# Optimization experiments

Measured on AMD Instinct MI355X. Metric: run time of the kernel, lower is better.

Reference implementation:

```python
import jax, jax.numpy as jnp
import numpy as np

N_HEAD = 16
N_KV = 4
HEAD_DIM = 128
WINDOW = 1024
SINK = 4
THETA = 10000.0


def _rope_cos_sin(T, dim, theta, dtype):
    inv_freq = 1.0 / (theta ** (jnp.arange(0, dim, 2, dtype=jnp.float32) / dim))
    t = jnp.arange(T, dtype=jnp.float32)
    ang = jnp.outer(t, inv_freq)  # [T, dim/2]
    return jnp.cos(ang).astype(dtype), jnp.sin(ang).astype(dtype)


def _apply_rope(x, cos, sin):
    # x: [B, H, T, D]; cos/sin: [T, D/2]
    d2 = x.shape[-1] // 2
    x1, x2 = x[..., :d2], x[..., d2:]
    return jnp.concatenate([x1 * cos - x2 * sin, x2 * cos + x1 * sin], axis=-1)


def setup_inputs() -> dict:
    key = jax.random.key(0)
    ks = jax.random.split(key, 5)
    B, T, C = 2, 2048, 2048
    x = jax.random.normal(ks[0], (B, T, C), dtype=jnp.float32)
    s = 0.02
    wq = jax.random.normal(ks[1], (C, C), dtype=jnp.float32) * s
    wk = jax.random.normal(ks[2], (N_KV * HEAD_DIM, C), dtype=jnp.float32) * s
    wv = jax.random.normal(ks[3], (N_KV * HEAD_DIM, C), dtype=jnp.float32) * s
    wo = jax.random.normal(ks[4], (C, C), dtype=jnp.float32) * s
    return {"x": x, "wq": wq, "wk": wk, "wv": wv, "wo": wo}


def reference(x, wq, wk, wv, wo):
    B, T, C = x.shape
    # QKV projections (Linear with weight [out, in], no bias)
    q = (x @ wq.T).reshape(B, T, N_HEAD, HEAD_DIM).transpose(0, 2, 1, 3)  # [B,H,T,D]
    k = (x @ wk.T).reshape(B, T, N_KV, HEAD_DIM).transpose(0, 2, 1, 3)    # [B,Hkv,T,D]
    v = (x @ wv.T).reshape(B, T, N_KV, HEAD_DIM).transpose(0, 2, 1, 3)

    cos, sin = _rope_cos_sin(T, HEAD_DIM, THETA, x.dtype)
    q = _apply_rope(q, cos, sin)
    k = _apply_rope(k, cos, sin)

    # GQA: repeat kv heads to match query heads (repeat_interleave on head dim)
    rep = N_HEAD // N_KV
    k = jnp.repeat(k, rep, axis=1)
    v = jnp.repeat(v, rep, axis=1)

    # causal + sliding window + attention sink mask
    i = jnp.arange(T)[:, None]
    j = jnp.arange(T)[None, :]
    allowed = (j <= i) & (((i - j) <= WINDOW) | (j < SINK))
    bias = jnp.where(allowed, 0.0, -jnp.inf).astype(x.dtype)  # [T,T]

    scale = 1.0 / np.sqrt(HEAD_DIM)
    att = jnp.einsum("bhqd,bhkd->bhqk", q, k) * scale + bias
    att = jax.nn.softmax(att, axis=-1)
    y = jnp.einsum("bhqk,bhkd->bhqd", att, v)  # [B,H,T,D]
    y = y.transpose(0, 2, 1, 3).reshape(B, T, C)
    return y @ wo.T
```

## Files before the change

### kernel.cpp

```cpp
#include <hip/hip_runtime.h>
#include <hip/hip_bf16.h>

typedef __bf16 bf16x8 __attribute__((ext_vector_type(8)));
typedef __bf16 bf16x4 __attribute__((ext_vector_type(4)));
typedef float  f32x4  __attribute__((ext_vector_type(4)));
typedef unsigned int uint4v __attribute__((ext_vector_type(4)));

#define NB     2
#define TT     2048
#define CC     2048
#define NH     16
#define NKV    4
#define HD     128
#define WIN    1024
#define SINKN  4
#define QSCALE 0.08838834764831845f

__device__ __forceinline__ void lds_load16(const void* g, void* l) {
    __builtin_amdgcn_global_load_lds(
        (__attribute__((address_space(1))) void*)const_cast<void*>(g),
        (__attribute__((address_space(3))) void*)l, 16, 0, 0);
}

__device__ __forceinline__ unsigned pack2bf(float a, float b) {
    __bf16 x = (__bf16)a, y = (__bf16)b;
    unsigned short ux = __builtin_bit_cast(unsigned short, x);
    unsigned short uy = __builtin_bit_cast(unsigned short, y);
    return (unsigned)ux | ((unsigned)uy << 16);
}

__global__ void cvt_kernel(const float* __restrict__ in, __bf16* __restrict__ out, int n) {
    int idx = (blockIdx.x * blockDim.x + threadIdx.x) * 4;
    const int stride = gridDim.x * blockDim.x * 4;
    for (; idx < n; idx += stride) {
        const float4 v = *(const float4*)(in + idx);
        bf16x4 o;
        o[0] = (__bf16)v.x; o[1] = (__bf16)v.y; o[2] = (__bf16)v.z; o[3] = (__bf16)v.w;
        *(bf16x4*)(out + idx) = o;
    }
}

__global__ void cvt_w_kernel(const float* __restrict__ wq, const float* __restrict__ wk,
                             const float* __restrict__ wv, const float* __restrict__ wo,
                             __bf16* __restrict__ out) {
    int idx = (blockIdx.x * blockDim.x + threadIdx.x) * 4;
    const int stride = gridDim.x * blockDim.x * 4;
    for (; idx < 10485760; idx += stride) {
        const float* src; int off;
        if (idx < 4194304)      { src = wq; off = idx; }
        else if (idx < 5242880) { src = wk; off = idx - 4194304; }
        else if (idx < 6291456) { src = wv; off = idx - 5242880; }
        else                    { src = wo; off = idx - 6291456; }
        const float4 v = *(const float4*)(src + off);
        bf16x4 o;
        o[0] = (__bf16)v.x; o[1] = (__bf16)v.y; o[2] = (__bf16)v.z; o[3] = (__bf16)v.w;
        *(bf16x4*)(out + idx) = o;
    }
}

__global__ void rope_table_kernel(float* __restrict__ cosT, float* __restrict__ sinT) {
    const int i = blockIdx.x * blockDim.x + threadIdx.x;
    const int t = i >> 6, d = i & 63;
    const float inv_freq = 1.0f / powf(10000.0f, (float)d * (1.0f / 64.0f));
    const float ang = (float)t * inv_freq;
    cosT[i] = cosf(ang);
    sinT[i] = sinf(ang);
}

__global__ void rope_scatter_kernel(const __bf16* __restrict__ qkv,
                                    const float* __restrict__ cosT,
                                    const float* __restrict__ sinT,
                                    __bf16* __restrict__ Qo,
                                    __bf16* __restrict__ Ko) {
    const int m = blockIdx.x;
    const int b = m >> 11, t = m & 2047;
    const __bf16* row = qkv + (size_t)m * 3072;
    for (int p = threadIdx.x; p < 1280; p += 256) {
        const int d = p & 63;
        const float c = cosT[t * 64 + d], s = sinT[t * 64 + d];
        if (p < 1024) {
            const int hh = p >> 6;
            const float x1 = (float)row[hh * 128 + d];
            const float x2 = (float)row[hh * 128 + d + 64];
            __bf16* o = Qo + ((size_t)(b * NH + hh) * TT + t) * HD;
            o[d]      = (__bf16)((x1 * c - x2 * s) * QSCALE);
            o[d + 64] = (__bf16)((x2 * c + x1 * s) * QSCALE);
        } else {
            const int g = (p - 1024) >> 6;
            const float x1 = (float)row[2048 + g * 128 + d];
            const float x2 = (float)row[2048 + g * 128 + d + 64];
            __bf16* o = Ko + ((size_t)(b * NKV + g) * TT + t) * HD;
            o[d]      = (__bf16)(x1 * c - x2 * s);
            o[d + 64] = (__bf16)(x2 * c + x1 * s);
        }
    }
}

__global__ void v_transpose_kernel(const __bf16* __restrict__ qkv, __bf16* __restrict__ Vt) {
    __shared__ __bf16 tile[64][72];
    const int bkv = blockIdx.z;
    const int b = bkv >> 2, g = bkv & 3;
    const int t0 = blockIdx.x << 6, d0 = blockIdx.y << 6;
    const int r = threadIdx.x >> 2, cg = threadIdx.x & 3;
    const __bf16* src = qkv + (size_t)(b * TT + t0 + r) * 3072 + 2560 + g * 128 + d0 + cg * 16;
    *(bf16x8*)&tile[r][cg * 16]     = *(const bf16x8*)src;
    *(bf16x8*)&tile[r][cg * 16 + 8] = *(const bf16x8*)(src + 8);
    __syncthreads();
    __bf16* dst = Vt + ((size_t)bkv * HD + d0 + r) * TT + t0 + cg * 16;
    bf16x8 o0, o1;
#pragma unroll
    for (int c2 = 0; c2 < 8; ++c2) {
        o0[c2] = tile[cg * 16 + c2][r];
        o1[c2] = tile[cg * 16 + 8 + c2][r];
    }
    *(bf16x8*)dst = o0;
    *(bf16x8*)(dst + 8) = o1;
}

template <int OUT_BF16>
__global__ __launch_bounds__(512, 2) void gemm_bt8(const __bf16* __restrict__ A,
                                                   const __bf16* __restrict__ Bm,
                                                   void* __restrict__ C,
                                                   int M, int N, int K) {
    __shared__ __align__(16) __bf16 lA[2][256 * 64];
    __shared__ __align__(16) __bf16 lB[2][256 * 64];
    const int tid = threadIdx.x;
    const int lane = tid & 63;
    const int w = tid >> 6;
    const int wm = w >> 2, wn = w & 3;
    const int nbn = N >> 8;
    const int bm = blockIdx.x / nbn, bn = blockIdx.x % nbn;
    const int m0 = bm << 8, n0 = bn << 8;
    const int lr = lane & 15, lh = lane >> 4;
    const int NT = K >> 6;

    auto stageA = [&](int kt, int buf, int i) {
        const int d = i * 8192 + tid * 16;
        const int row = d >> 7;
        const int colb = (d & 127) ^ ((row & 7) << 4);
        lds_load16(A + (size_t)(m0 + row) * K + kt * 64 + (colb >> 1),
                   (char*)lA[buf] + i * 8192 + w * 1024);
    };
    auto stageB = [&](int kt, int buf, int i) {
        const int d = i * 8192 + tid * 16;
        const int row = d >> 7;
        const int colb = (d & 127) ^ ((row & 7) << 4);
        lds_load16(Bm + (size_t)(n0 + row) * K + kt * 64 + (colb >> 1),
                   (char*)lB[buf] + i * 8192 + w * 1024);
    };

    f32x4 acc[8][4] = {};

#pragma unroll
    for (int i = 0; i < 4; ++i) stageA(0, 0, i);
#pragma unroll
    for (int i = 0; i < 4; ++i) stageB(0, 0, i);
    asm volatile("s_waitcnt vmcnt(0)" ::: "memory");
    __syncthreads();

    for (int kt = 0; kt < NT; ++kt) {
        const int cur = kt & 1, nxt = cur ^ 1;
        const bool pf = (kt + 1 < NT);
        const char* bA = (const char*)lA[cur];
        const char* bB = (const char*)lB[cur];

        bf16x8 aF[4][2], b0[2][2], b1[2][2];
#pragma unroll
        for (int mf = 0; mf < 4; ++mf)
#pragma unroll
            for (int ks = 0; ks < 2; ++ks) {
                const int row = wm * 128 + mf * 16 + lr;
                const int cb = (ks * 64 + lh * 16) ^ ((row & 7) << 4);
                aF[mf][ks] = *(const bf16x8*)(bA + row * 128 + cb);
            }
#pragma unroll
        for (int nf = 0; nf < 2; ++nf)
#pragma unroll
            for (int ks = 0; ks < 2; ++ks) {
                const int row = wn * 64 + nf * 16 + lr;
                const int cb = (ks * 64 + lh * 16) ^ ((row & 7) << 4);
                b0[nf][ks] = *(const bf16x8*)(bB + row * 128 + cb);
            }
        if (pf) { stageA(kt + 1, nxt, 0); stageA(kt + 1, nxt, 1); stageA(kt + 1, nxt, 2); stageA(kt + 1, nxt, 3); }
        __builtin_amdgcn_s_setprio(1);
#pragma unroll
        for (int mf = 0; mf < 4; ++mf)
#pragma unroll
            for (int nf = 0; nf < 2; ++nf)
#pragma unroll
                for (int ks = 0; ks < 2; ++ks)
                    acc[mf][nf] = __builtin_amdgcn_mfma_f32_16x16x32_bf16(aF[mf][ks], b0[nf][ks], acc[mf][nf], 0, 0, 0);
        __builtin_amdgcn_s_setprio(0);

#pragma unroll
        for (int nf = 0; nf < 2; ++nf)
#pragma unroll
            for (int ks = 0; ks < 2; ++ks) {
                const int row = wn * 64 + 32 + nf * 16 + lr;
                const int cb = (ks * 64 + lh * 16) ^ ((row & 7) << 4);
                b1[nf][ks] = *(const bf16x8*)(bB + row * 128 + cb);
            }
        if (pf) { stageB(kt + 1, nxt, 0); stageB(kt + 1, nxt, 1); stageB(kt + 1, nxt, 2); stageB(kt + 1, nxt, 3); }
        __builtin_amdgcn_s_setprio(1);
#pragma unroll
        for (int mf = 0; mf < 4; ++mf)
#pragma unroll
            for (int nf = 0; nf < 2; ++nf)
#pragma unroll
                for (int ks = 0; ks < 2; ++ks)
                    acc[mf][nf + 2] = __builtin_amdgcn_mfma_f32_16x16x32_bf16(aF[mf][ks], b1[nf][ks], acc[mf][nf + 2], 0, 0, 0);
        __builtin_amdgcn_s_setprio(0);

#pragma unroll
        for (int mf = 0; mf < 4; ++mf)
#pragma unroll
            for (int ks = 0; ks < 2; ++ks) {
                const int row = wm * 128 + 64 + mf * 16 + lr;
                const int cb = (ks * 64 + lh * 16) ^ ((row & 7) << 4);
                aF[mf][ks] = *(const bf16x8*)(bA + row * 128 + cb);
            }
        __builtin_amdgcn_s_setprio(1);
#pragma unroll
        for (int mf = 0; mf < 4; ++mf)
#pragma unroll
            for (int nf = 0; nf < 2; ++nf)
#pragma unroll
                for (int ks = 0; ks < 2; ++ks)
                    acc[mf + 4][nf] = __builtin_amdgcn_mfma_f32_16x16x32_bf16(aF[mf][ks], b0[nf][ks], acc[mf + 4][nf], 0, 0, 0);
        __builtin_amdgcn_s_setprio(0);

        __builtin_amdgcn_s_setprio(1);
#pragma unroll
        for (int mf = 0; mf < 4; ++mf)
#pragma unroll
            for (int nf = 0; nf < 2; ++nf)
#pragma unroll
                for (int ks = 0; ks < 2; ++ks)
                    acc[mf + 4][nf + 2] = __builtin_amdgcn_mfma_f32_16x16x32_bf16(aF[mf][ks], b1[nf][ks], acc[mf + 4][nf + 2], 0, 0, 0);
        __builtin_amdgcn_s_setprio(0);

        asm volatile("s_waitcnt vmcnt(0)" ::: "memory");
        __syncthreads();
    }

#pragma unroll
    for (int mf = 0; mf < 8; ++mf)
#pragma unroll
        for (int nf = 0; nf < 4; ++nf)
#pragma unroll
            for (int r = 0; r < 4; ++r) {
                const size_t row = m0 + wm * 128 + mf * 16 + lh * 4 + r;
                const size_t col = n0 + wn * 64 + nf * 16 + lr;
                if (OUT_BF16) ((__bf16*)C)[row * N + col] = (__bf16)acc[mf][nf][r];
                else          ((float*)C)[row * N + col]  = acc[mf][nf][r];
            }
}

template <int OUT_BF16>
__global__ __launch_bounds__(256, 2) void gemm_bt(const __bf16* __restrict__ A,
                                                  const __bf16* __restrict__ Bm,
                                                  void* __restrict__ C,
                                                  int M, int N, int K) {
    __shared__ __align__(16) __bf16 lA[128 * 32];
    __shared__ __align__(16) __bf16 lB[128 * 32];
    const int tid = threadIdx.x;
    const int lane = tid & 63;
    const int w = tid >> 6;
    const int wr = w >> 1, wc = w & 1;
    const int nbn = N >> 7;
    const int bm = blockIdx.x / nbn, bn = blockIdx.x % nbn;
    const int m0 = bm << 7, n0 = bn << 7;
    const int lr = lane & 15, lk = (lane >> 4) << 3;
    f32x4 acc[4][4] = {};

    for (int k0 = 0; k0 < K; k0 += 32) {
        __syncthreads();
#pragma unroll
        for (int L = 0; L < 2; ++L) {
            const int o = L * 4096 + w * 1024 + lane * 16;
            const int row = o >> 6, col = (o & 63) >> 1;
            lds_load16(A + (size_t)(m0 + row) * K + k0 + col, (char*)lA + L * 4096 + w * 1024);
            lds_load16(Bm + (size_t)(n0 + row) * K + k0 + col, (char*)lB + L * 4096 + w * 1024);
        }
        asm volatile("s_waitcnt vmcnt(0)" ::: "memory");
        __syncthreads();

        bf16x8 af[4], bfr[4];
#pragma unroll
        for (int t = 0; t < 4; ++t) {
            af[t]  = *(const bf16x8*)&lA[(wr * 64 + t * 16 + lr) * 32 + lk];
            bfr[t] = *(const bf16x8*)&lB[(wc * 64 + t * 16 + lr) * 32 + lk];
        }
#pragma unroll
        for (int mt = 0; mt < 4; ++mt)
#pragma unroll
            for (int nt = 0; nt < 4; ++nt)
                acc[mt][nt] = __builtin_amdgcn_mfma_f32_16x16x32_bf16(af[mt], bfr[nt], acc[mt][nt], 0, 0, 0);
    }

    const int r0 = (lane >> 4) * 4;
#pragma unroll
    for (int mt = 0; mt < 4; ++mt)
#pragma unroll
        for (int nt = 0; nt < 4; ++nt)
#pragma unroll
            for (int r = 0; r < 4; ++r) {
                const size_t row = m0 + wr * 64 + mt * 16 + r0 + r;
                const size_t col = n0 + wc * 64 + nt * 16 + lr;
                if (OUT_BF16) ((__bf16*)C)[row * N + col] = (__bf16)acc[mt][nt][r];
                else          ((float*)C)[row * N + col]  = acc[mt][nt][r];
            }
}

__global__ __launch_bounds__(512, 4) void attn_kernel(const __bf16* __restrict__ Q,
                                                      const __bf16* __restrict__ Kg,
                                                      const __bf16* __restrict__ Vt,
                                                      __bf16* __restrict__ Y) {
    const int qt2 = 63 - blockIdx.x;
    const int kv = blockIdx.y, b = blockIdx.z;
    const int q0 = qt2 << 5;
    const int tid = threadIdx.x, lane = tid & 63, w = tid >> 6;
    const int lr = lane & 15, lh = lane >> 4;
    const int hh = w >> 1;
    const int h  = kv * 4 + hh;
    const int wh = w & 1;

    __shared__ __align__(16) __bf16 lK[64 * 128];
    __shared__ __align__(16) __bf16 lV[128 * 64];

    bf16x8 qf[4];
    {
        const __bf16* Qb = Q + ((size_t)(b * NH + h) * TT + q0 + wh * 16) * HD;
#pragma unroll
        for (int kc = 0; kc < 4; ++kc)
            qf[kc] = *(const bf16x8*)(Qb + lr * HD + kc * 32 + lh * 8);
    }

    f32x4 acc[8] = {};
    float mrun = -1e30f, lrun = 0.f;
    const int iq = q0 + wh * 16 + lr;

    const __bf16* Kb = Kg + (size_t)(b * NKV + kv) * TT * HD;
    const __bf16* Vb = Vt + (size_t)(b * NKV + kv) * HD * TT;
    const int jend = qt2 >> 1;
    const int jsw  = (q0 > WIN) ? ((q0 - WIN) >> 6) : 0;

    for (int jb = 0; jb <= jend; ++jb) {
        if (jb > 0 && jb < jsw) continue;
        const int j0 = jb << 6;
        __syncthreads();
#pragma unroll
        for (int L = 0; L < 2; ++L) {
            const int o = L * 8192 + w * 1024 + lane * 16;
            {
                const int row = o >> 8;
                const int colb = (o & 255) ^ ((row & 7) << 4);
                lds_load16(Kb + (size_t)(j0 + row) * HD + (colb >> 1), (char*)lK + L * 8192 + w * 1024);
            }
            {
                const int row = o >> 7;
                const int colb = (o & 127) ^ ((row & 7) << 4);
                lds_load16(Vb + (size_t)row * TT + j0 + (colb >> 1), (char*)lV + L * 8192 + w * 1024);
            }
        }
        asm volatile("s_waitcnt vmcnt(0)" ::: "memory");
        __syncthreads();

        f32x4 s4[4];
#pragma unroll
        for (int nt = 0; nt < 4; ++nt) {
            f32x4 s = {0.f, 0.f, 0.f, 0.f};
#pragma unroll
            for (int kc = 0; kc < 4; ++kc) {
                const int row = nt * 16 + lr;
                const int colb = ((kc * 32 + lh * 8) << 1) ^ ((row & 7) << 4);
                const bf16x8 kf = *(const bf16x8*)((const char*)lK + row * 256 + colb);
                s = __builtin_amdgcn_mfma_f32_16x16x32_bf16(kf, qf[kc], s, 0, 0, 0);
            }
            s4[nt] = s;
        }

        const bool fullTile = (j0 + 63 <= q0) && (q0 + 31 - j0 <= WIN);
        if (!fullTile) {
#pragma unroll
            for (int nt = 0; nt < 4; ++nt)
#pragma unroll
                for (int r = 0; r < 4; ++r) {
                    const int j = j0 + nt * 16 + lh * 4 + r;
                    const bool ok = (j <= iq) && ((iq - j <= WIN) || (j < SINKN));
                    if (!ok) s4[nt][r] = -1e30f;
                }
        }

        float mx = s4[0][0];
#pragma unroll
        for (int nt = 0; nt < 4; ++nt)
#pragma unroll
            for (int r = 0; r < 4; ++r) mx = fmaxf(mx, s4[nt][r]);
        mx = fmaxf(mx, __shfl_xor(mx, 16, 64));
        mx = fmaxf(mx, __shfl_xor(mx, 32, 64));

        if (!__all(mx - mrun <= 8.0f)) {
            const float mnew = fmaxf(mrun, mx);
            const float corr = __expf(mrun - mnew);
            mrun = mnew;
            lrun *= corr;
#pragma unroll
            for (int r = 0; r < 4; ++r) {
                const float c = __shfl(corr, lh * 4 + r, 64);
#pragma unroll
                for (int dt = 0; dt < 8; ++dt) acc[dt][r] *= c;
            }
        }

        float rsum = 0.f;
#pragma unroll
        for (int nt = 0; nt < 4; ++nt)
#pragma unroll
            for (int r = 0; r < 4; ++r) {
                const float p = __expf(s4[nt][r] - mrun);
                s4[nt][r] = p;
                rsum += p;
            }
        rsum += __shfl_xor(rsum, 16, 64);
        rsum += __shfl_xor(rsum, 32, 64);
        lrun += rsum;

        unsigned pw[4][2];
#pragma unroll
        for (int nt = 0; nt < 4; ++nt) {
            pw[nt][0] = pack2bf(s4[nt][0], s4[nt][1]);
            pw[nt][1] = pack2bf(s4[nt][2], s4[nt][3]);
        }
        bf16x8 pa[2];
#pragma unroll
        for (int kc = 0; kc < 2; ++kc) {
            uint4v wv;
#pragma unroll
            for (int widx = 0; widx < 4; ++widx) {
                const int m = widx & 1;
                const int srcl = lr + 16 * ((2 * lh + (widx >> 1)) & 3);
                const int wA = __shfl((int)pw[2 * kc][m], srcl, 64);
                const int wB = __shfl((int)pw[2 * kc + 1][m], srcl, 64);
                wv[widx] = (unsigned)((lh & 2) ? wB : wA);
            }
            pa[kc] = __builtin_bit_cast(bf16x8, wv);
        }

#pragma unroll
        for (int dt = 0; dt < 8; ++dt) {
#pragma unroll
            for (int kc = 0; kc < 2; ++kc) {
                const int row = dt * 16 + lr;
                const int colb = ((kc * 32 + lh * 8) << 1) ^ ((row & 7) << 4);
                const bf16x8 vf = *(const bf16x8*)((const char*)lV + row * 128 + colb);
                acc[dt] = __builtin_amdgcn_mfma_f32_16x16x32_bf16(pa[kc], vf, acc[dt], 0, 0, 0);
            }
        }
    }

    const float inv = 1.f / lrun;
#pragma unroll
    for (int r = 0; r < 4; ++r) {
        const float invr = __shfl(inv, lh * 4 + r, 64);
        const int trow = q0 + wh * 16 + lh * 4 + r;
        __bf16* Yp = Y + ((size_t)b * TT + trow) * CC + h * HD;
#pragma unroll
        for (int dt = 0; dt < 8; ++dt)
            Yp[dt * 16 + lr] = (__bf16)(acc[dt][r] * invr);
    }
}

extern "C" void kernel_launch(void* const* d_in, const int* in_sizes, int n_in,
                              void* d_out, int out_size, void* d_ws, size_t ws_size,
                              hipStream_t stream) {
    const float* x  = (const float*)d_in[0];
    const float* wq = (const float*)d_in[1];
    const float* wk = (const float*)d_in[2];
    const float* wv = (const float*)d_in[3];
    const float* wo = (const float*)d_in[4];
    float* out = (float*)d_out;

    char* ws = (char*)d_ws;
    size_t off = 0;
    auto alloc = [&](size_t bytes) { char* p = ws + off; off += bytes; return p; };
    __bf16* xb   = (__bf16*)alloc(16777216);
    __bf16* Wall = (__bf16*)alloc(12582912);
    __bf16* wob  = (__bf16*)alloc(8388608);
    __bf16* qkv  = (__bf16*)alloc(25165824);
    __bf16* Qs   = (__bf16*)alloc(16777216);
    __bf16* Ks   = (__bf16*)alloc(4194304);
    __bf16* Vts  = (__bf16*)alloc(4194304);
    float*  cosT = (float*)alloc(524288);
    float*  sinT = (float*)alloc(524288);
    __bf16* Yb = xb;

    cvt_kernel<<<2048, 256, 0, stream>>>(x, xb, 4096 * 2048);
    cvt_w_kernel<<<2048, 256, 0, stream>>>(wq, wk, wv, wo, Wall);
    rope_table_kernel<<<512, 256, 0, stream>>>(cosT, sinT);

    gemm_bt8<1><<<dim3(16 * 12), 512, 0, stream>>>(xb, Wall, qkv, 4096, 3072, 2048);
    rope_scatter_kernel<<<4096, 256, 0, stream>>>(qkv, cosT, sinT, Qs, Ks);
    v_transpose_kernel<<<dim3(32, 2, 8), 256, 0, stream>>>(qkv, Vts);
    attn_kernel<<<dim3(64, 4, 2), 512, 0, stream>>>(Qs, Ks, Vts, Yb);
    gemm_bt<0><<<dim3(32 * 16), 256, 0, stream>>>(Yb, wob, out, 4096, 2048, 2048);
}
```

Measured before the change: 196.9 us.

## Vectorize RoPE scatter, double-buffer output GEMM, widen attention KV tiles

The RoPE scatter kernel now gives each thread 8 contiguous elements and uses 16-byte vector loads and stores in place of scalar accesses. The output-projection GEMM double-buffers its LDS tiles so the next K-slice load overlaps the current MFMA work. The attention kernel processes 128-key tiles instead of 64, halving the number of loop iterations and barriers. The cost is more LDS per block (64KB in attention) and coarser masking and window skipping, which may lower occupancy and waste work at tile boundaries.

```diff
diff --git a/kernel.cpp b/kernel.cpp
--- a/kernel.cpp
+++ b/kernel.cpp
@@ -72,28 +72,45 @@
                                     const float* __restrict__ sinT,
                                     __bf16* __restrict__ Qo,
                                     __bf16* __restrict__ Ko) {
-    const int m = blockIdx.x;
-    const int b = m >> 11, t = m & 2047;
-    const __bf16* row = qkv + (size_t)m * 3072;
-    for (int p = threadIdx.x; p < 1280; p += 256) {
-        const int d = p & 63;
-        const float c = cosT[t * 64 + d], s = sinT[t * 64 + d];
-        if (p < 1024) {
-            const int hh = p >> 6;
-            const float x1 = (float)row[hh * 128 + d];
-            const float x2 = (float)row[hh * 128 + d + 64];
-            __bf16* o = Qo + ((size_t)(b * NH + hh) * TT + t) * HD;
-            o[d]      = (__bf16)((x1 * c - x2 * s) * QSCALE);
-            o[d + 64] = (__bf16)((x2 * c + x1 * s) * QSCALE);
-        } else {
-            const int g = (p - 1024) >> 6;
-            const float x1 = (float)row[2048 + g * 128 + d];
-            const float x2 = (float)row[2048 + g * 128 + d + 64];
-            __bf16* o = Ko + ((size_t)(b * NKV + g) * TT + t) * HD;
-            o[d]      = (__bf16)(x1 * c - x2 * s);
-            o[d + 64] = (__bf16)(x2 * c + x1 * s);
-        }
-    }
+    const int job = blockIdx.x * 256 + threadIdx.x;
+    int m, d8, base_off; __bf16* outp; float scale;
+    if (job < 524288) {
+        m = job >> 7;
+        const int pj = job & 127;
+        const int hh = pj >> 3; d8 = pj & 7;
+        base_off = hh * 128;
+        const int b = m >> 11, t = m & 2047;
+        outp = Qo + ((size_t)(b * NH + hh) * TT + t) * HD + d8 * 8;
+        scale = QSCALE;
+    } else {
+        const int j2 = job - 524288;
+        m = j2 >> 5;
+        const int pj = j2 & 31;
+        const int g = pj >> 3; d8 = pj & 7;
+        base_off = 2048 + g * 128;
+        const int b = m >> 11, t = m & 2047;
+        outp = Ko + ((size_t)(b * NKV + g) * TT + t) * HD + d8 * 8;
+        scale = 1.0f;
+    }
+    const int t = m & 2047;
+    const __bf16* row = qkv + (size_t)m * 3072 + base_off + d8 * 8;
+    const bf16x8 x1 = *(const bf16x8*)row;
+    const bf16x8 x2 = *(const bf16x8*)(row + 64);
+    const float4 c0 = *(const float4*)(cosT + t * 64 + d8 * 8);
+    const float4 c1 = *(const float4*)(cosT + t * 64 + d8 * 8 + 4);
+    const float4 s0 = *(const float4*)(sinT + t * 64 + d8 * 8);
+    const float4 s1 = *(const float4*)(sinT + t * 64 + d8 * 8 + 4);
+    const float cs[8] = {c0.x, c0.y, c0.z, c0.w, c1.x, c1.y, c1.z, c1.w};
+    const float sn[8] = {s0.x, s0.y, s0.z, s0.w, s1.x, s1.y, s1.z, s1.w};
+    bf16x8 o1, o2;
+#pragma unroll
+    for (int e = 0; e < 8; ++e) {
+        const float a = (float)x1[e], bb = (float)x2[e];
+        o1[e] = (__bf16)((a * cs[e] - bb * sn[e]) * scale);
+        o2[e] = (__bf16)((bb * cs[e] + a * sn[e]) * scale);
+    }
+    *(bf16x8*)outp = o1;
+    *(bf16x8*)(outp + 64) = o2;
 }
 
 __global__ void v_transpose_kernel(const __bf16* __restrict__ qkv, __bf16* __restrict__ Vt) {
@@ -261,8 +278,8 @@
                                                   const __bf16* __restrict__ Bm,
                                                   void* __restrict__ C,
                                                   int M, int N, int K) {
-    __shared__ __align__(16) __bf16 lA[128 * 32];
-    __shared__ __align__(16) __bf16 lB[128 * 32];
+    __shared__ __align__(16) __bf16 lA[2][128 * 32];
+    __shared__ __align__(16) __bf16 lB[2][128 * 32];
     const int tid = threadIdx.x;
     const int lane = tid & 63;
     const int w = tid >> 6;
@@ -273,29 +290,39 @@
     const int lr = lane & 15, lk = (lane >> 4) << 3;
     f32x4 acc[4][4] = {};
 
-    for (int k0 = 0; k0 < K; k0 += 32) {
-        __syncthreads();
+    auto stage = [&](int k0, int buf) {
 #pragma unroll
         for (int L = 0; L < 2; ++L) {
             const int o = L * 4096 + w * 1024 + lane * 16;
             const int row = o >> 6, col = (o & 63) >> 1;
-            lds_load16(A + (size_t)(m0 + row) * K + k0 + col, (char*)lA + L * 4096 + w * 1024);
-            lds_load16(Bm + (size_t)(n0 + row) * K + k0 + col, (char*)lB + L * 4096 + w * 1024);
-        }
+            lds_load16(A + (size_t)(m0 + row) * K + k0 + col, (char*)lA[buf] + L * 4096 + w * 1024);
+            lds_load16(Bm + (size_t)(n0 + row) * K + k0 + col, (char*)lB[buf] + L * 4096 + w * 1024);
+        }
+    };
+
+    stage(0, 0);
+    asm volatile("s_waitcnt vmcnt(0)" ::: "memory");
+    __syncthreads();
+
+    const int NT = K >> 5;
+    for (int kt = 0; kt < NT; ++kt) {
+        const int buf = kt & 1;
+        if (kt + 1 < NT) stage((kt + 1) << 5, buf ^ 1);
+
+        bf16x8 af[4], bfr[4];
+#pragma unroll
+        for (int t = 0; t < 4; ++t) {
+            af[t]  = *(const bf16x8*)&lA[buf][(wr * 64 + t * 16 + lr) * 32 + lk];
+            bfr[t] = *(const bf16x8*)&lB[buf][(wc * 64 + t * 16 + lr) * 32 + lk];
+        }
+#pragma unroll
+        for (int mt = 0; mt < 4; ++mt)
+#pragma unroll
+            for (int nt = 0; nt < 4; ++nt)
+                acc[mt][nt] = __builtin_amdgcn_mfma_f32_16x16x32_bf16(af[mt], bfr[nt], acc[mt][nt], 0, 0, 0);
+
         asm volatile("s_waitcnt vmcnt(0)" ::: "memory");
         __syncthreads();
-
-        bf16x8 af[4], bfr[4];
-#pragma unroll
-        for (int t = 0; t < 4; ++t) {
-            af[t]  = *(const bf16x8*)&lA[(wr * 64 + t * 16 + lr) * 32 + lk];
-            bfr[t] = *(const bf16x8*)&lB[(wc * 64 + t * 16 + lr) * 32 + lk];
-        }
-#pragma unroll
-        for (int mt = 0; mt < 4; ++mt)
-#pragma unroll
-            for (int nt = 0; nt < 4; ++nt)
-                acc[mt][nt] = __builtin_amdgcn_mfma_f32_16x16x32_bf16(af[mt], bfr[nt], acc[mt][nt], 0, 0, 0);
     }
 
     const int r0 = (lane >> 4) * 4;
@@ -325,8 +352,8 @@
     const int h  = kv * 4 + hh;
     const int wh = w & 1;
 
-    __shared__ __align__(16) __bf16 lK[64 * 128];
-    __shared__ __align__(16) __bf16 lV[128 * 64];
+    __shared__ __align__(16) __bf16 lK[128 * 128];
+    __shared__ __align__(16) __bf16 lV[128 * 128];
 
     bf16x8 qf[4];
     {
@@ -342,33 +369,27 @@
 
     const __bf16* Kb = Kg + (size_t)(b * NKV + kv) * TT * HD;
     const __bf16* Vb = Vt + (size_t)(b * NKV + kv) * HD * TT;
-    const int jend = qt2 >> 1;
-    const int jsw  = (q0 > WIN) ? ((q0 - WIN) >> 6) : 0;
+    const int jend = (q0 + 31) >> 7;
+    const int jsw  = (q0 > WIN) ? ((q0 - WIN) >> 7) : 0;
 
     for (int jb = 0; jb <= jend; ++jb) {
         if (jb > 0 && jb < jsw) continue;
-        const int j0 = jb << 6;
+        const int j0 = jb << 7;
         __syncthreads();
 #pragma unroll
-        for (int L = 0; L < 2; ++L) {
+        for (int L = 0; L < 4; ++L) {
             const int o = L * 8192 + w * 1024 + lane * 16;
-            {
-                const int row = o >> 8;
-                const int colb = (o & 255) ^ ((row & 7) << 4);
-                lds_load16(Kb + (size_t)(j0 + row) * HD + (colb >> 1), (char*)lK + L * 8192 + w * 1024);
-            }
-            {
-                const int row = o >> 7;
-                const int colb = (o & 127) ^ ((row & 7) << 4);
-                lds_load16(Vb + (size_t)row * TT + j0 + (colb >> 1), (char*)lV + L * 8192 + w * 1024);
-            }
+            const int row = o >> 8;
+            const int colb = (o & 255) ^ ((row & 7) << 4);
+            lds_load16(Kb + (size_t)(j0 + row) * HD + (colb >> 1), (char*)lK + L * 8192 + w * 1024);
+            lds_load16(Vb + (size_t)row * TT + j0 + (colb >> 1), (char*)lV + L * 8192 + w * 1024);
         }
         asm volatile("s_waitcnt vmcnt(0)" ::: "memory");
         __syncthreads();
 
-        f32x4 s4[4];
-#pragma unroll
-        for (int nt = 0; nt < 4; ++nt) {
+        f32x4 s4[8];
+#pragma unroll
+        for (int nt = 0; nt < 8; ++nt) {
             f32x4 s = {0.f, 0.f, 0.f, 0.f};
 #pragma unroll
             for (int kc = 0; kc < 4; ++kc) {
@@ -380,10 +401,10 @@
             s4[nt] = s;
         }
 
-        const bool fullTile = (j0 + 63 <= q0) && (q0 + 31 - j0 <= WIN);
+        const bool fullTile = (j0 + 127 <= q0) && (q0 + 31 - j0 <= WIN);
         if (!fullTile) {
 #pragma unroll
-            for (int nt = 0; nt < 4; ++nt)
+            for (int nt = 0; nt < 8; ++nt)
 #pragma unroll
                 for (int r = 0; r < 4; ++r) {
                     const int j = j0 + nt * 16 + lh * 4 + r;
@@ -394,7 +415,7 @@
 
         float mx = s4[0][0];
 #pragma unroll
-        for (int nt = 0; nt < 4; ++nt)
+        for (int nt = 0; nt < 8; ++nt)
 #pragma unroll
             for (int r = 0; r < 4; ++r) mx = fmaxf(mx, s4[nt][r]);
         mx = fmaxf(mx, __shfl_xor(mx, 16, 64));
@@ -415,7 +436,7 @@
 
         float rsum = 0.f;
 #pragma unroll
-        for (int nt = 0; nt < 4; ++nt)
+        for (int nt = 0; nt < 8; ++nt)
 #pragma unroll
             for (int r = 0; r < 4; ++r) {
                 const float p = __expf(s4[nt][r] - mrun);
@@ -426,15 +447,15 @@
         rsum += __shfl_xor(rsum, 32, 64);
         lrun += rsum;
 
-        unsigned pw[4][2];
-#pragma unroll
-        for (int nt = 0; nt < 4; ++nt) {
+        unsigned pw[8][2];
+#pragma unroll
+        for (int nt = 0; nt < 8; ++nt) {
             pw[nt][0] = pack2bf(s4[nt][0], s4[nt][1]);
             pw[nt][1] = pack2bf(s4[nt][2], s4[nt][3]);
         }
-        bf16x8 pa[2];
-#pragma unroll
-        for (int kc = 0; kc < 2; ++kc) {
+        bf16x8 pa[4];
+#pragma unroll
+        for (int kc = 0; kc < 4; ++kc) {
             uint4v wv;
 #pragma unroll
             for (int widx = 0; widx < 4; ++widx) {
@@ -450,10 +471,10 @@
 #pragma unroll
         for (int dt = 0; dt < 8; ++dt) {
 #pragma unroll
-            for (int kc = 0; kc < 2; ++kc) {
+            for (int kc = 0; kc < 4; ++kc) {
                 const int row = dt * 16 + lr;
                 const int colb = ((kc * 32 + lh * 8) << 1) ^ ((row & 7) << 4);
-                const bf16x8 vf = *(const bf16x8*)((const char*)lV + row * 128 + colb);
+                const bf16x8 vf = *(const bf16x8*)((const char*)lV + row * 256 + colb);
                 acc[dt] = __builtin_amdgcn_mfma_f32_16x16x32_bf16(pa[kc], vf, acc[dt], 0, 0, 0);
             }
         }
@@ -500,7 +521,7 @@
     rope_table_kernel<<<512, 256, 0, stream>>>(cosT, sinT);
 
     gemm_bt8<1><<<dim3(16 * 12), 512, 0, stream>>>(xb, Wall, qkv, 4096, 3072, 2048);
-    rope_scatter_kernel<<<4096, 256, 0, stream>>>(qkv, cosT, sinT, Qs, Ks);
+    rope_scatter_kernel<<<2560, 256, 0, stream>>>(qkv, cosT, sinT, Qs, Ks);
     v_transpose_kernel<<<dim3(32, 2, 8), 256, 0, stream>>>(qkv, Vts);
     attn_kernel<<<dim3(64, 4, 2), 512, 0, stream>>>(Qs, Ks, Vts, Yb);
     gemm_bt<0><<<dim3(32 * 16), 256, 0, stream>>>(Yb, wob, out, 4096, 2048, 2048);
```

After: 220.6 us. +12.0%, slower.
